# Kernel tuning notes

Measured on AMD Instinct MI355X. Metric: run time of the kernel, lower is better.

## Reference

```python
import jax, jax.numpy as jnp
import numpy as np

L = 8          # context_length
P = 196        # patches_per_frame
PT = 16        # patches_per_tactile_frame
N_EMBD = 768
N_HEAD = 12
BATCH = 4
T = (L + 1) + L * PT + L * P  # 1705


def build_mask(L, P, Pt):
    # image-query block rows (L*P rows)
    mi = np.zeros((L * P, L * P))
    a1 = np.zeros((L * P, L + 1))
    t1 = np.zeros((L * P, L * Pt))
    for i in range(L):
        mi[i * P:(i + 1) * P, :(i + 1) * P] = 1
        a1[i * P:(i + 2) * P, :i + 2] = 1
        t1[i * P:(i + 1) * P, :(i + 1) * Pt] = 1
    m1 = np.concatenate([a1, t1, mi], axis=1)
    # tactile-query block rows (L*Pt rows)
    a2 = np.zeros((L * Pt, L + 1))
    t2 = np.zeros((L * Pt, L * Pt))
    i2 = np.zeros((L * Pt, L * P))
    for i in range(L):
        a2[i * Pt:(i + 2) * Pt, :i + 2] = 1
        t2[i * Pt:(i + 1) * Pt, :(i + 1) * Pt] = 1
        i2[i * Pt:(i + 1) * Pt, :(i + 1) * P] = 1
    m2 = np.concatenate([a2, t2, i2], axis=1)
    # action-query rows (L+1 rows)
    a3 = np.zeros((L + 1, L + 1))
    t3 = np.zeros((L + 1, L * Pt))
    i3 = np.zeros((L + 1, L * P))
    for i in range(L + 1):
        a3[i:i + 2, :i + 2] = 1
        t3[i:i + 1, :(i + 1) * Pt] = 1
        i3[i:i + 1, :(i + 1) * P] = 1
    m3 = np.concatenate([a3, t3, i3], axis=1)
    return np.concatenate([m3, m2, m1], axis=0).astype(bool)


def setup_inputs() -> dict:
    key = jax.random.key(0)
    k1, k2, k3 = jax.random.split(key, 3)
    x = jax.random.normal(k1, (BATCH, T, N_EMBD), dtype=jnp.float32)
    W_attn = jax.random.normal(k2, (N_EMBD, 3 * N_EMBD), dtype=jnp.float32) * 0.02
    W_proj = jax.random.normal(k3, (N_EMBD, N_EMBD), dtype=jnp.float32) * 0.02
    mask = jnp.asarray(build_mask(L, P, PT))
    return {"x": x, "W_attn": W_attn, "W_proj": W_proj, "mask": mask, "n_head": N_HEAD}


def reference(x, W_attn, W_proj, mask, n_head):
    B, Tq, C = x.shape
    hd = C // n_head
    qkv = x @ W_attn                      # [B, T, 3C]
    q, k, v = jnp.split(qkv, 3, axis=-1)
    # [B, H, T, hd]
    q = q.reshape(B, Tq, n_head, hd).transpose(0, 2, 1, 3)
    k = k.reshape(B, Tq, n_head, hd).transpose(0, 2, 1, 3)
    v = v.reshape(B, Tq, n_head, hd).transpose(0, 2, 1, 3)
    scores = jnp.einsum("bhqd,bhkd->bhqk", q, k) / jnp.sqrt(jnp.float32(hd))
    scores = jnp.where(mask[None, None, :, :], scores, jnp.float32(-1e9))
    probs = jax.nn.softmax(scores, axis=-1)
    y = jnp.einsum("bhqk,bhkd->bhqd", probs, v)
    y = y.transpose(0, 2, 1, 3).reshape(B, Tq, C)
    return y @ W_proj
```

## Files before the change

### kernel.cpp

```cpp
#include <hip/hip_runtime.h>
#include <hip/hip_bf16.h>

typedef __attribute__((ext_vector_type(8))) short short8;
typedef __attribute__((ext_vector_type(4))) float f32x4;

#define MFMA16(a,b,c) __builtin_amdgcn_mfma_f32_16x16x32_bf16((a),(b),(c),0,0,0)

#define WAITVM4_BAR() asm volatile("s_waitcnt vmcnt(4)\n\ts_barrier" ::: "memory")
#define WAITVM3_BAR() asm volatile("s_waitcnt vmcnt(3)\n\ts_barrier" ::: "memory")
#define WAITVM0_BAR() asm volatile("s_waitcnt vmcnt(0)\n\ts_barrier" ::: "memory")
#define LG0_BAR()     asm volatile("s_waitcnt lgkmcnt(0)\n\ts_barrier" ::: "memory")

constexpr int Tt = 1705;
constexpr int Tp = 1792;
constexpr int NKT_ALL = 28;
constexpr int NH = 12, HD = 64, Bb = 4, C_ = 768;
constexpr int M_  = Bb * Tt;
constexpr int Mp  = 6912;
constexpr int NQT = 14;
constexpr int NCH = 4;
constexpr float QSCALE = 0.18033688011116016f;

static_assert(C_ % 64 == 0, "K-loop assumes K % 64 == 0");

__device__ __forceinline__ void gl16(const void* g, void* l) {
  __builtin_amdgcn_global_load_lds((const __attribute__((address_space(1))) void*)g,
                                   (__attribute__((address_space(3))) void*)l, 16, 0, 0);
}

__device__ __forceinline__ float ex2(float x) {
  float r; asm("v_exp_f32 %0, %1" : "=v"(r) : "v"(x)); return r;
}

__device__ __forceinline__ int frame_of(int t) {
  return t < 9 ? t : (t < 137 ? ((t - 9) >> 4) : ((t - 137) / 196));
}

__device__ __forceinline__ int lim16(int a) {
  if (a >= Tt) return 0;
  int bnd = min(a + 15, Tt - 1);
  int fmax = (a == 0) ? 8 : frame_of(min(bnd, a < 137 ? 136 : bnd));
  return (fmax >= 8) ? Tt : 137 + (fmax + 1) * 196;
}

__global__ __launch_bounds__(256) void k_conv_x(const float* __restrict__ x,
                                                __hip_bfloat16* __restrict__ xb) {
  int i = blockIdx.x * 256 + threadIdx.x;
  if (i >= Mp * C_ / 4) return;
  float4 v = make_float4(0.f, 0.f, 0.f, 0.f);
  if (i * 4 < M_ * C_) v = ((const float4*)x)[i];
  __hip_bfloat16 o0 = __float2bfloat16(v.x), o1 = __float2bfloat16(v.y),
                 o2 = __float2bfloat16(v.z), o3 = __float2bfloat16(v.w);
  ushort4 u = make_ushort4(*(unsigned short*)&o0, *(unsigned short*)&o1,
                           *(unsigned short*)&o2, *(unsigned short*)&o3);
  ((ushort4*)xb)[i] = u;
}

__global__ __launch_bounds__(256) void k_transpose_w(const float* __restrict__ src,
                                                     __hip_bfloat16* __restrict__ dst,
                                                     int K, int N) {
  __shared__ float tile[32][33];
  int kb = blockIdx.x * 32, nb = blockIdx.y * 32;
  int tx = threadIdx.x & 31, ty = threadIdx.x >> 5;
  for (int i = 0; i < 4; i++)
    tile[ty + i * 8][tx] = src[(size_t)(kb + ty + i * 8) * N + nb + tx];
  __syncthreads();
  for (int i = 0; i < 4; i++)
    dst[(size_t)(nb + ty + i * 8) * K + kb + tx] = __float2bfloat16(tile[tx][ty + i * 8]);
}

__device__ __forceinline__ void stage128(const __hip_bfloat16* A, const __hip_bfloat16* Bt,
                                         int K, int m0, int n0, int k0,
                                         __hip_bfloat16* As, __hip_bfloat16* Bs) {
  const int tid = threadIdx.x;
  for (int rr = 0; rr < 2; rr++) {
    int idx = rr * 256 + tid;
    int row = idx >> 2;
    int c8 = (idx & 3) ^ ((row >> 1) & 3);
    gl16(A  + (size_t)(m0 + row) * K + k0 + c8 * 8, As + idx * 8);
    gl16(Bt + (size_t)(n0 + row) * K + k0 + c8 * 8, Bs + idx * 8);
  }
}

__device__ __forceinline__ void compute128(const __hip_bfloat16* As, const __hip_bfloat16* Bs,
                                           int wy, int wx, int l16, int grp,
                                           f32x4 acc[4][4]) {
  short8 a[4], b[4];
  for (int i = 0; i < 4; i++) {
    int row = wy * 64 + i * 16 + l16;
    a[i] = *(const short8*)(As + row * 32 + ((grp ^ ((row >> 1) & 3)) * 8));
  }
  for (int j = 0; j < 4; j++) {
    int row = wx * 64 + j * 16 + l16;
    b[j] = *(const short8*)(Bs + row * 32 + ((grp ^ ((row >> 1) & 3)) * 8));
  }
  for (int i = 0; i < 4; i++)
    for (int j = 0; j < 4; j++)
      acc[i][j] = MFMA16(a[i], b[j], acc[i][j]);
}

__device__ __forceinline__ void gemm_tile_bt(const __hip_bfloat16* A,
                                             const __hip_bfloat16* Bt,
                                             int K, int m0, int n0,
                                             __hip_bfloat16* As0, __hip_bfloat16* Bs0,
                                             __hip_bfloat16* As1, __hip_bfloat16* Bs1,
                                             f32x4 acc[4][4]) {
  const int lane = threadIdx.x & 63, w = threadIdx.x >> 6;
  const int wy = w >> 1, wx = w & 1;
  const int l16 = lane & 15, grp = lane >> 4;
  for (int i = 0; i < 4; i++)
    for (int j = 0; j < 4; j++) { f32x4 z = {0.f,0.f,0.f,0.f}; acc[i][j] = z; }
  const int NP = K >> 6;
  stage128(A, Bt, K, m0, n0, 0, As0, Bs0);
  for (int p = 0; p < NP; p++) {
    int k0 = p << 6;
    stage128(A, Bt, K, m0, n0, k0 + 32, As1, Bs1);
    WAITVM4_BAR();
    compute128(As0, Bs0, wy, wx, l16, grp, acc);
    LG0_BAR();
    if (p + 1 < NP) {
      stage128(A, Bt, K, m0, n0, k0 + 64, As0, Bs0);
      WAITVM4_BAR();
    } else {
      WAITVM0_BAR();
    }
    compute128(As1, Bs1, wy, wx, l16, grp, acc);
    LG0_BAR();
  }
}

__global__ __launch_bounds__(256) void k_gemm_qkv(const __hip_bfloat16* __restrict__ xb,
                                                  const __hip_bfloat16* __restrict__ wat,
                                                  __hip_bfloat16* __restrict__ q,
                                                  __hip_bfloat16* __restrict__ kpk,
                                                  __hip_bfloat16* __restrict__ vpk) {
  __shared__ __hip_bfloat16 As0[128 * 32], Bs0[128 * 32];
  __shared__ __hip_bfloat16 As1[128 * 32], Bs1[128 * 32];
  f32x4 acc[4][4];
  int m0 = blockIdx.x * 128, n0 = blockIdx.y * 128;
  gemm_tile_bt(xb, wat, C_, m0, n0, As0, Bs0, As1, Bs1, acc);
  const int lane = threadIdx.x & 63, w = threadIdx.x >> 6;
  const int wy = w >> 1, wx = w & 1;
  const int l16 = lane & 15, grp = lane >> 4;
  for (int i = 0; i < 4; i++)
    for (int r = 0; r < 4; r++) {
      int m = m0 + wy * 64 + i * 16 + grp * 4 + r;
      if (m >= M_) continue;
      int b = m / Tt, t = m - b * Tt;
      for (int j = 0; j < 4; j++) {
        int n = n0 + wx * 64 + j * 16 + l16;
        int which = n / C_;
        int c = n - which * C_;
        int h = c >> 6, d = c & 63;
        float val = acc[i][j][r];
        int bh = b * NH + h;
        if (which == 0) {
          q[((size_t)bh * Tp + t) * HD + d] = __float2bfloat16(val * QSCALE);
        } else if (which == 1) {
          int kt = t >> 6, jj = (t >> 4) & 3, mm = t & 15;
          int half = d >> 5, gg = (d >> 3) & 3, ss = d & 7;
          kpk[(((size_t)bh * NKT_ALL + kt) * 8 + jj * 2 + half) * 512 +
              (gg * 16 + mm) * 8 + ss] = __float2bfloat16(val);
        } else {
          int kt = t >> 6, kb2 = (t >> 5) & 1, k32 = t & 31;
          int gg = (k32 >> 2) & 3, ss = (k32 & 3) + ((k32 >> 4) & 1) * 4;
          int jt = d >> 4, mm = d & 15;
          vpk[(((size_t)bh * NKT_ALL + kt) * 8 + jt * 2 + kb2) * 512 +
              (gg * 16 + mm) * 8 + ss] = __float2bfloat16(val);
        }
      }
    }
}

__global__ __launch_bounds__(256) void k_gemm_proj64(const __hip_bfloat16* __restrict__ A,
                                                     const __hip_bfloat16* __restrict__ Bt,
                                                     float* __restrict__ out) {
  __shared__ __hip_bfloat16 As0[64 * 32], Bs0[128 * 32];
  __shared__ __hip_bfloat16 As1[64 * 32], Bs1[128 * 32];
  const int tid = threadIdx.x;
  const int lane = tid & 63, w = tid >> 6;
  const int l16 = lane & 15, grp = lane >> 4;
  const int m0 = blockIdx.x * 64, n0 = blockIdx.y * 128;
  f32x4 acc[8];
  for (int j = 0; j < 8; j++) { f32x4 z = {0.f,0.f,0.f,0.f}; acc[j] = z; }

  auto stage = [&](int k0, __hip_bfloat16* As, __hip_bfloat16* Bs) {
    int row = tid >> 2;
    int c8 = (tid & 3) ^ ((row >> 1) & 3);
    gl16(A + (size_t)(m0 + row) * C_ + k0 + c8 * 8, As + tid * 8);
    for (int rr = 0; rr < 2; rr++) {
      int idx = rr * 256 + tid;
      int brow = idx >> 2;
      int bc8 = (idx & 3) ^ ((brow >> 1) & 3);
      gl16(Bt + (size_t)(n0 + brow) * C_ + k0 + bc8 * 8, Bs + idx * 8);
    }
  };
  auto comp = [&](const __hip_bfloat16* As, const __hip_bfloat16* Bs) {
    int arow = w * 16 + l16;
    short8 a = *(const short8*)(As + arow * 32 + ((grp ^ ((arow >> 1) & 3)) * 8));
    for (int j = 0; j < 8; j++) {
      int brow = j * 16 + l16;
      short8 b = *(const short8*)(Bs + brow * 32 + ((grp ^ ((brow >> 1) & 3)) * 8));
      acc[j] = MFMA16(a, b, acc[j]);
    }
  };

  constexpr int NP = C_ >> 6;
  stage(0, As0, Bs0);
  for (int p = 0; p < NP; p++) {
    int k0 = p << 6;
    stage(k0 + 32, As1, Bs1);
    WAITVM3_BAR();
    comp(As0, Bs0);
    LG0_BAR();
    if (p + 1 < NP) {
      stage(k0 + 64, As0, Bs0);
      WAITVM3_BAR();
    } else {
      WAITVM0_BAR();
    }
    comp(As1, Bs1);
    LG0_BAR();
  }

  for (int r = 0; r < 4; r++) {
    int m = m0 + w * 16 + grp * 4 + r;
    if (m >= M_) continue;
    for (int j = 0; j < 8; j++)
      out[(size_t)m * C_ + n0 + j * 16 + l16] = acc[j][r];
  }
}

union S8u { short8 v; struct { unsigned long long lo, hi; } q; unsigned u[4]; };

__device__ __forceinline__ unsigned pack2bf(float a, float b) {
  union { __hip_bfloat162 h; unsigned u; } cv;
  cv.h = __float22bfloat162_rn(make_float2(a, b));
  return cv.u;
}

__global__ __launch_bounds__(256, 2) void k_attn(const __hip_bfloat16* __restrict__ q,
                                                 const __hip_bfloat16* __restrict__ kpk,
                                                 const __hip_bfloat16* __restrict__ vpk,
                                                 __hip_bfloat16* __restrict__ Opart,
                                                 float* __restrict__ lpart) {
  const int tid = threadIdx.x, lane = tid & 63, w = tid >> 6;
  const int l16 = lane & 15, grp = lane >> 4;
  const int id = blockIdx.x;
  const int xslot = id & 7, rr_ = id >> 3;
  const int bh = xslot + 8 * (rr_ / 56);
  const int cq = rr_ % 56;
  const int qt = cq >> 2, ch = cq & (NCH - 1);
  const int t0q = qt * 128;
  const __hip_bfloat16* qb = q + (size_t)bh * Tp * HD;

  int lim[2], Cmn[2], Ath[2], Bth[2], Cth[2];
  for (int g = 0; g < 2; g++) {
    int a = t0q + w * 32 + g * 16;
    lim[g] = lim16(a);
    int fqmn, fql;
    if (a >= Tt) { fqmn = 8; fql = 8; }
    else {
      int bnd = min(a + 15, Tt - 1);
      fqmn = min(frame_of(a), frame_of(bnd));
      int t = a + l16;
      fql = (t >= Tt) ? 8 : frame_of(t);
    }
    Cmn[g] = min(137 + 196 * (fqmn + 1), Tt);
    Ath[g] = fql + 2;
    Bth[g] = 9 + 16 * (fql + 1);
    Cth[g] = min(137 + 196 * (fql + 1), Tt);
  }
  int limw = max(lim[0], lim[1]);
  int nktw = (limw + 63) >> 6;
  int k0t = (ch * nktw) >> 2;
  int k1t = ((ch + 1) * nktw) >> 2;

  short8 qa[2][2];
  for (int g = 0; g < 2; g++) {
    const __hip_bfloat16* qr = qb + (size_t)(t0q + w * 32 + g * 16 + l16) * HD + grp * 8;
    qa[g][0] = *(const short8*)(qr);
    qa[g][1] = *(const short8*)(qr + 32);
  }
  f32x4 o[2][4];
  for (int g = 0; g < 2; g++)
    for (int jt = 0; jt < 4; jt++) { f32x4 z = {0.f,0.f,0.f,0.f}; o[g][jt] = z; }
  f32x4 ps[2];
  { f32x4 z = {0.f,0.f,0.f,0.f}; ps[0] = z; ps[1] = z; }

  const short8* kbase = (const short8*)(kpk + (size_t)bh * NKT_ALL * 4096);
  const short8* vbase = (const short8*)(vpk + (size_t)bh * NKT_ALL * 4096);

  for (int kt = k0t; kt < k1t; kt++) {
    const int t0k = kt * 64;
    const short8* kp = kbase + (size_t)kt * 512;
    const short8* vp = vbase + (size_t)kt * 512;
    short8 kf[4][2], vf[4][2];
    for (int j = 0; j < 4; j++)
      for (int hh = 0; hh < 2; hh++) kf[j][hh] = kp[(j * 2 + hh) * 64 + lane];
    for (int jt = 0; jt < 4; jt++)
      for (int kb2 = 0; kb2 < 2; kb2++) vf[jt][kb2] = vp[(jt * 2 + kb2) * 64 + lane];

    f32x4 s[2][4];
    for (int j = 0; j < 4; j++) {
      f32x4 z = {0.f,0.f,0.f,0.f};
      s[0][j] = MFMA16(kf[j][0], qa[0][0], z);
      s[0][j] = MFMA16(kf[j][1], qa[0][1], s[0][j]);
      s[1][j] = MFMA16(kf[j][0], qa[1][0], z);
      s[1][j] = MFMA16(kf[j][1], qa[1][1], s[1][j]);
    }

    bool act0 = t0k < lim[0], act1 = t0k < lim[1];
    bool fullk = (t0k + 64 <= Tt);
    S8u pf[2][2];
    for (int g = 0; g < 2; g++) {
      bool act = g == 0 ? act0 : act1;
      if (!act) continue;
      bool needm = !(fullk && (t0k >= 192 ? (t0k + 64) <= Cmn[g] : Cmn[g] >= Tt));
      if (needm) {
        for (int j = 0; j < 4; j++)
          for (int r = 0; r < 4; r++) {
            int key = t0k + j * 16 + grp * 4 + r;
            int thr = key < 9 ? Ath[g] : (key < 137 ? Bth[g] : Cth[g]);
            if (key >= thr) s[g][j][r] = -1e30f;
          }
      }
      f32x4 p[4];
      for (int j = 0; j < 4; j++)
        for (int r = 0; r < 4; r++) p[j][r] = ex2(s[g][j][r]);
      ps[g] += (p[0] + p[1]) + (p[2] + p[3]);
      pf[g][0].u[0] = pack2bf(p[0][0], p[0][1]);
      pf[g][0].u[1] = pack2bf(p[0][2], p[0][3]);
      pf[g][0].u[2] = pack2bf(p[1][0], p[1][1]);
      pf[g][0].u[3] = pack2bf(p[1][2], p[1][3]);
      pf[g][1].u[0] = pack2bf(p[2][0], p[2][1]);
      pf[g][1].u[1] = pack2bf(p[2][2], p[2][3]);
      pf[g][1].u[2] = pack2bf(p[3][0], p[3][1]);
      pf[g][1].u[3] = pack2bf(p[3][2], p[3][3]);
    }

    for (int jt = 0; jt < 4; jt++)
      for (int kb2 = 0; kb2 < 2; kb2++) {
        if (act0) o[0][jt] = MFMA16(vf[jt][kb2], pf[0][kb2].v, o[0][jt]);
        if (act1) o[1][jt] = MFMA16(vf[jt][kb2], pf[1][kb2].v, o[1][jt]);
      }
  }

  float lr[2];
  for (int g = 0; g < 2; g++) {
    float sum = (ps[g][0] + ps[g][1]) + (ps[g][2] + ps[g][3]);
    sum += __shfl_xor(sum, 16);
    sum += __shfl_xor(sum, 32);
    lr[g] = sum;
  }

  const int blk = bh * (NQT * NCH) + cq;
  __hip_bfloat16* op = Opart + (size_t)blk * (128 * 64);
  for (int g = 0; g < 2; g++) {
    int row = w * 32 + g * 16 + l16;
    for (int jt = 0; jt < 4; jt++) {
      unsigned p01 = pack2bf(o[g][jt][0], o[g][jt][1]);
      unsigned p23 = pack2bf(o[g][jt][2], o[g][jt][3]);
      ushort4 u;
      u.x = p01 & 0xffff; u.y = p01 >> 16; u.z = p23 & 0xffff; u.w = p23 >> 16;
      *(ushort4*)(op + row * 64 + jt * 16 + grp * 4) = u;
    }
    if (grp == 0) lpart[(size_t)blk * 128 + w * 32 + g * 16 + l16] = lr[g];
  }
}

__global__ __launch_bounds__(256) void k_combine(const __hip_bfloat16* __restrict__ Opart,
                                                 const float* __restrict__ lpart,
                                                 __hip_bfloat16* __restrict__ y) {
  const int tid = threadIdx.x;
  const int qt = blockIdx.x, bh = blockIdx.y;
  const int b = bh / NH, h = bh - b * NH;
  const int t0q = qt * 128;
  const int blk0 = bh * (NQT * NCH) + qt * NCH;
  __shared__ float ls[128];
  if (tid < 128) {
    float s = 0.f;
    for (int c = 0; c < NCH; c++) s += lpart[(size_t)(blk0 + c) * 128 + tid];
    ls[tid] = (s > 0.f) ? 1.0f / s : 0.f;
  }
  __syncthreads();
  for (int it = 0; it < 4; it++) {
    int e8 = it * 256 + tid;
    int e = e8 * 8;
    int row = e >> 6, d = e & 63;
    int t = t0q + row;
    if (t >= Tt) continue;
    float acc[8] = {0,0,0,0,0,0,0,0};
    for (int c = 0; c < NCH; c++) {
      short8 vv = *(const short8*)(Opart + (size_t)(blk0 + c) * (128 * 64) + e);
      for (int i = 0; i < 8; i++) {
        union { unsigned u; float f; } cv;
        cv.u = ((unsigned)(unsigned short)vv[i]) << 16;
        acc[i] += cv.f;
      }
    }
    float rinv = ls[row];
    short8 outv;
    for (int i = 0; i < 8; i += 2) {
      unsigned p = pack2bf(acc[i] * rinv, acc[i + 1] * rinv);
      outv[i] = (short)(p & 0xffff);
      outv[i + 1] = (short)(p >> 16);
    }
    *(short8*)(y + (size_t)(b * Tt + t) * C_ + h * 64 + d) = outv;
  }
}

extern "C" void kernel_launch(void* const* d_in, const int* in_sizes, int n_in,
                              void* d_out, int out_size, void* d_ws, size_t ws_size,
                              hipStream_t stream) {
  const float* x  = (const float*)d_in[0];
  const float* Wa = (const float*)d_in[1];
  const float* Wp = (const float*)d_in[2];
  float* out = (float*)d_out;

  char* ws = (char*)d_ws;
  size_t off = 0;
  auto alloc = [&](size_t bytes) { size_t r = off; off += (bytes + 255) & ~(size_t)255; return r; };
  __hip_bfloat16* xb  = (__hip_bfloat16*)(ws + alloc((size_t)Mp * C_ * 2));
  __hip_bfloat16* wat = (__hip_bfloat16*)(ws + alloc((size_t)3 * C_ * C_ * 2));
  __hip_bfloat16* wpt = (__hip_bfloat16*)(ws + alloc((size_t)C_ * C_ * 2));
  __hip_bfloat16* qb  = (__hip_bfloat16*)(ws + alloc((size_t)Bb * NH * Tp * HD * 2));
  __hip_bfloat16* kpk = (__hip_bfloat16*)(ws + alloc((size_t)Bb * NH * NKT_ALL * 4096 * 2));
  __hip_bfloat16* vpk = (__hip_bfloat16*)(ws + alloc((size_t)Bb * NH * NKT_ALL * 4096 * 2));
  __hip_bfloat16* yb  = (__hip_bfloat16*)(ws + alloc((size_t)Mp * C_ * 2));
  __hip_bfloat16* Opart = (__hip_bfloat16*)(ws + alloc((size_t)Bb * NH * NQT * NCH * 128 * 64 * 2));
  float*          lpart = (float*)(ws + alloc((size_t)Bb * NH * NQT * NCH * 128 * 4));

  k_conv_x<<<(Mp * C_ / 4 + 255) / 256, 256, 0, stream>>>(x, xb);
  k_transpose_w<<<dim3(C_ / 32, 3 * C_ / 32), 256, 0, stream>>>(Wa, wat, C_, 3 * C_);
  k_transpose_w<<<dim3(C_ / 32, C_ / 32), 256, 0, stream>>>(Wp, wpt, C_, C_);
  k_gemm_qkv<<<dim3(Mp / 128, 3 * C_ / 128), 256, 0, stream>>>(xb, wat, qb, kpk, vpk);
  k_attn<<<dim3(Bb * NH * NQT * NCH), 256, 0, stream>>>(qb, kpk, vpk, Opart, lpart);
  k_combine<<<dim3(NQT, Bb * NH), 256, 0, stream>>>(Opart, lpart, yb);
  k_gemm_proj64<<<dim3(Mp / 64, C_ / 128), 256, 0, stream>>>(yb, wpt, out);
}
```

Baseline: 222.7 us.

## Enlarge QKV GEMM to 256x256 tiles with 8 waves and double-buffered pipeline

Rewrites the QKV projection GEMM to use 256x256 output tiles per 512-thread block, with each wave computing 128x64 instead of 64x64. The K loop becomes a single 32-wide double-buffered stage, with prefetch split into two passes around the MFMA halves and s_setprio raised during MFMA bursts. The larger tiles increase operand reuse from LDS and global memory and cut the block count. In exchange the grid shrinks to 27x9 = 243 blocks, which leaves some CUs idle. The higher register pressure from 128 accumulator floats per lane may also limit occupancy.

```diff
diff --git a/kernel.cpp b/kernel.cpp
--- a/kernel.cpp
+++ b/kernel.cpp
@@ -6,7 +6,6 @@
 
 #define MFMA16(a,b,c) __builtin_amdgcn_mfma_f32_16x16x32_bf16((a),(b),(c),0,0,0)
 
-#define WAITVM4_BAR() asm volatile("s_waitcnt vmcnt(4)\n\ts_barrier" ::: "memory")
 #define WAITVM3_BAR() asm volatile("s_waitcnt vmcnt(3)\n\ts_barrier" ::: "memory")
 #define WAITVM0_BAR() asm volatile("s_waitcnt vmcnt(0)\n\ts_barrier" ::: "memory")
 #define LG0_BAR()     asm volatile("s_waitcnt lgkmcnt(0)\n\ts_barrier" ::: "memory")
@@ -21,7 +20,7 @@
 constexpr int NCH = 4;
 constexpr float QSCALE = 0.18033688011116016f;
 
-static_assert(C_ % 64 == 0, "K-loop assumes K % 64 == 0");
+static_assert(Mp % 256 == 0 && (3 * C_) % 256 == 0, "256-tile grid");
 
 __device__ __forceinline__ void gl16(const void* g, void* l) {
   __builtin_amdgcn_global_load_lds((const __attribute__((address_space(1))) void*)g,
@@ -69,90 +68,79 @@
     dst[(size_t)(nb + ty + i * 8) * K + kb + tx] = __float2bfloat16(tile[tx][ty + i * 8]);
 }
 
-__device__ __forceinline__ void stage128(const __hip_bfloat16* A, const __hip_bfloat16* Bt,
-                                         int K, int m0, int n0, int k0,
-                                         __hip_bfloat16* As, __hip_bfloat16* Bs) {
-  const int tid = threadIdx.x;
-  for (int rr = 0; rr < 2; rr++) {
-    int idx = rr * 256 + tid;
-    int row = idx >> 2;
-    int c8 = (idx & 3) ^ ((row >> 1) & 3);
-    gl16(A  + (size_t)(m0 + row) * K + k0 + c8 * 8, As + idx * 8);
-    gl16(Bt + (size_t)(n0 + row) * K + k0 + c8 * 8, Bs + idx * 8);
-  }
-}
-
-__device__ __forceinline__ void compute128(const __hip_bfloat16* As, const __hip_bfloat16* Bs,
-                                           int wy, int wx, int l16, int grp,
-                                           f32x4 acc[4][4]) {
-  short8 a[4], b[4];
-  for (int i = 0; i < 4; i++) {
-    int row = wy * 64 + i * 16 + l16;
-    a[i] = *(const short8*)(As + row * 32 + ((grp ^ ((row >> 1) & 3)) * 8));
-  }
-  for (int j = 0; j < 4; j++) {
-    int row = wx * 64 + j * 16 + l16;
-    b[j] = *(const short8*)(Bs + row * 32 + ((grp ^ ((row >> 1) & 3)) * 8));
-  }
-  for (int i = 0; i < 4; i++)
-    for (int j = 0; j < 4; j++)
-      acc[i][j] = MFMA16(a[i], b[j], acc[i][j]);
-}
-
-__device__ __forceinline__ void gemm_tile_bt(const __hip_bfloat16* A,
-                                             const __hip_bfloat16* Bt,
-                                             int K, int m0, int n0,
-                                             __hip_bfloat16* As0, __hip_bfloat16* Bs0,
-                                             __hip_bfloat16* As1, __hip_bfloat16* Bs1,
-                                             f32x4 acc[4][4]) {
-  const int lane = threadIdx.x & 63, w = threadIdx.x >> 6;
-  const int wy = w >> 1, wx = w & 1;
-  const int l16 = lane & 15, grp = lane >> 4;
-  for (int i = 0; i < 4; i++)
-    for (int j = 0; j < 4; j++) { f32x4 z = {0.f,0.f,0.f,0.f}; acc[i][j] = z; }
-  const int NP = K >> 6;
-  stage128(A, Bt, K, m0, n0, 0, As0, Bs0);
-  for (int p = 0; p < NP; p++) {
-    int k0 = p << 6;
-    stage128(A, Bt, K, m0, n0, k0 + 32, As1, Bs1);
-    WAITVM4_BAR();
-    compute128(As0, Bs0, wy, wx, l16, grp, acc);
-    LG0_BAR();
-    if (p + 1 < NP) {
-      stage128(A, Bt, K, m0, n0, k0 + 64, As0, Bs0);
-      WAITVM4_BAR();
-    } else {
-      WAITVM0_BAR();
-    }
-    compute128(As1, Bs1, wy, wx, l16, grp, acc);
-    LG0_BAR();
-  }
-}
-
-__global__ __launch_bounds__(256) void k_gemm_qkv(const __hip_bfloat16* __restrict__ xb,
+__global__ __launch_bounds__(512) void k_gemm_qkv(const __hip_bfloat16* __restrict__ xb,
                                                   const __hip_bfloat16* __restrict__ wat,
                                                   __hip_bfloat16* __restrict__ q,
                                                   __hip_bfloat16* __restrict__ kpk,
                                                   __hip_bfloat16* __restrict__ vpk) {
-  __shared__ __hip_bfloat16 As0[128 * 32], Bs0[128 * 32];
-  __shared__ __hip_bfloat16 As1[128 * 32], Bs1[128 * 32];
-  f32x4 acc[4][4];
-  int m0 = blockIdx.x * 128, n0 = blockIdx.y * 128;
-  gemm_tile_bt(xb, wat, C_, m0, n0, As0, Bs0, As1, Bs1, acc);
-  const int lane = threadIdx.x & 63, w = threadIdx.x >> 6;
-  const int wy = w >> 1, wx = w & 1;
+  __shared__ __hip_bfloat16 As[2][256 * 32], Bs[2][256 * 32];
+  const int tid = threadIdx.x;
+  const int lane = tid & 63, w = tid >> 6;
+  const int wr = w >> 2, wc = w & 3;
   const int l16 = lane & 15, grp = lane >> 4;
-  for (int i = 0; i < 4; i++)
+  const int m0 = blockIdx.x * 256, n0 = blockIdx.y * 256;
+  constexpr int NT = C_ / 32;
+
+  auto stage_pass = [&](int t, int bb, int p) {
+    int idx = p * 512 + tid;
+    int row = idx >> 2;
+    int c8 = (idx & 3) ^ ((row >> 1) & 3);
+    int k0 = t * 32;
+    gl16(xb  + (size_t)(m0 + row) * C_ + k0 + c8 * 8, &As[bb][idx * 8]);
+    gl16(wat + (size_t)(n0 + row) * C_ + k0 + c8 * 8, &Bs[bb][idx * 8]);
+  };
+
+  f32x4 acc[8][4];
+  for (int i = 0; i < 8; i++)
+    for (int j = 0; j < 4; j++) { f32x4 z = {0.f,0.f,0.f,0.f}; acc[i][j] = z; }
+
+  stage_pass(0, 0, 0);
+  stage_pass(0, 0, 1);
+  WAITVM0_BAR();
+
+  for (int t = 0; t < NT; t++) {
+    const int cur = t & 1, nxt = cur ^ 1;
+    const __hip_bfloat16* Ac = As[cur];
+    const __hip_bfloat16* Bc = Bs[cur];
+    short8 bfr[4], afr[4];
+    if (t + 1 < NT) stage_pass(t + 1, nxt, 0);
+    for (int nj = 0; nj < 4; nj++) {
+      int row = wc * 64 + nj * 16 + l16;
+      bfr[nj] = *(const short8*)(Bc + row * 32 + ((grp ^ ((row >> 1) & 3)) * 8));
+    }
+    for (int mi = 0; mi < 4; mi++) {
+      int row = wr * 128 + mi * 16 + l16;
+      afr[mi] = *(const short8*)(Ac + row * 32 + ((grp ^ ((row >> 1) & 3)) * 8));
+    }
+    __builtin_amdgcn_s_setprio(1);
+    for (int mi = 0; mi < 4; mi++)
+      for (int nj = 0; nj < 4; nj++)
+        acc[mi][nj] = MFMA16(afr[mi], bfr[nj], acc[mi][nj]);
+    __builtin_amdgcn_s_setprio(0);
+    if (t + 1 < NT) stage_pass(t + 1, nxt, 1);
+    for (int mi = 0; mi < 4; mi++) {
+      int row = wr * 128 + 64 + mi * 16 + l16;
+      afr[mi] = *(const short8*)(Ac + row * 32 + ((grp ^ ((row >> 1) & 3)) * 8));
+    }
+    __builtin_amdgcn_s_setprio(1);
+    for (int mi = 0; mi < 4; mi++)
+      for (int nj = 0; nj < 4; nj++)
+        acc[4 + mi][nj] = MFMA16(afr[mi], bfr[nj], acc[4 + mi][nj]);
+    __builtin_amdgcn_s_setprio(0);
+    WAITVM0_BAR();
+  }
+
+  const int which = n0 / C_;
+  const int c0 = n0 - which * C_ + wc * 64;
+  for (int mi = 0; mi < 8; mi++)
     for (int r = 0; r < 4; r++) {
-      int m = m0 + wy * 64 + i * 16 + grp * 4 + r;
+      int m = m0 + wr * 128 + mi * 16 + grp * 4 + r;
       if (m >= M_) continue;
       int b = m / Tt, t = m - b * Tt;
-      for (int j = 0; j < 4; j++) {
-        int n = n0 + wx * 64 + j * 16 + l16;
-        int which = n / C_;
-        int c = n - which * C_;
+      for (int nj = 0; nj < 4; nj++) {
+        int c = c0 + nj * 16 + l16;
         int h = c >> 6, d = c & 63;
-        float val = acc[i][j][r];
+        float val = acc[mi][nj][r];
         int bh = b * NH + h;
         if (which == 0) {
           q[((size_t)bh * Tp + t) * HD + d] = __float2bfloat16(val * QSCALE);
@@ -434,7 +422,7 @@
   k_conv_x<<<(Mp * C_ / 4 + 255) / 256, 256, 0, stream>>>(x, xb);
   k_transpose_w<<<dim3(C_ / 32, 3 * C_ / 32), 256, 0, stream>>>(Wa, wat, C_, 3 * C_);
   k_transpose_w<<<dim3(C_ / 32, C_ / 32), 256, 0, stream>>>(Wp, wpt, C_, C_);
-  k_gemm_qkv<<<dim3(Mp / 128, 3 * C_ / 128), 256, 0, stream>>>(xb, wat, qb, kpk, vpk);
+  k_gemm_qkv<<<dim3(Mp / 256, 3 * C_ / 256), 512, 0, stream>>>(xb, wat, qb, kpk, vpk);
   k_attn<<<dim3(Bb * NH * NQT * NCH), 256, 0, stream>>>(qb, kpk, vpk, Opart, lpart);
   k_combine<<<dim3(NQT, Bb * NH), 256, 0, stream>>>(Opart, lpart, yb);
   k_gemm_proj64<<<dim3(Mp / 64, C_ / 128), 256, 0, stream>>>(yb, wpt, out);
```

Result: no change. 218.6 us (-1.8%).
